# Performance work log

Measured on AMD Instinct MI355X. Metric: run time of the kernel, lower is better.

The kernel has to match this reference:

```python
import jax, jax.numpy as jnp
import numpy as np

B, S, D = 4, 2048, 768
H = 12
HD = D // H  # 64


def setup_inputs() -> dict:
    key = jax.random.key(0)
    ks = jax.random.split(key, 9)
    scale = 0.02
    return {
        "hidden_states": jax.random.normal(ks[0], (B, S, D), dtype=jnp.float32),
        "Wq": jax.random.normal(ks[1], (D, D), dtype=jnp.float32) * scale,
        "bq": jnp.zeros((D,), dtype=jnp.float32),
        "Wk": jax.random.normal(ks[2], (D, D), dtype=jnp.float32) * scale,
        "bk": jnp.zeros((D,), dtype=jnp.float32),
        "Wv": jax.random.normal(ks[3], (D, D), dtype=jnp.float32) * scale,
        "bv": jnp.zeros((D,), dtype=jnp.float32),
        "Wo": jax.random.normal(ks[4], (D, D), dtype=jnp.float32) * scale,
        "bo": jnp.zeros((D,), dtype=jnp.float32),
    }


def reference(hidden_states, Wq, bq, Wk, bk, Wv, bv, Wo, bo):
    b, s, d = hidden_states.shape
    inv_sqrt_hd = 1.0 / jnp.sqrt(jnp.asarray(HD, dtype=hidden_states.dtype))

    def split_heads(x):  # [b, s, d] -> [b, h, s, hd]
        return x.reshape(b, s, H, HD).transpose(0, 2, 1, 3)

    q = split_heads(hidden_states @ Wq + bq)
    k = split_heads(hidden_states @ Wk + bk)
    v = split_heads(hidden_states @ Wv + bv)

    scores = jnp.einsum("bhqd,bhkd->bhqk", q, k) * inv_sqrt_hd
    probs = jax.nn.softmax(scores, axis=-1)
    ctx = jnp.einsum("bhqk,bhkd->bhqd", probs, v)  # [b, h, s, hd]
    ctx = ctx.transpose(0, 2, 1, 3).reshape(b, s, d)
    return ctx @ Wo + bo
```

## Files before the change

### kernel.cpp

```cpp
#include <hip/hip_runtime.h>

typedef unsigned short u16;
typedef __attribute__((ext_vector_type(4))) float f32x4;
typedef __attribute__((ext_vector_type(16))) float f32x16;
typedef __attribute__((ext_vector_type(8))) __bf16 bf16x8;
typedef __attribute__((ext_vector_type(8))) unsigned short u16x8;
typedef __attribute__((ext_vector_type(2))) unsigned u32x2;

#define L2E 1.44269504088896340736f

#if __has_builtin(__builtin_amdgcn_exp2f)
#define EXP2(x) __builtin_amdgcn_exp2f(x)
#else
#define EXP2(x) exp2f(x)
#endif

__device__ __forceinline__ u16 f2bf(float f) {
  unsigned u = __float_as_uint(f);
  u += 0x7fffu + ((u >> 16) & 1u);
  return (u16)(u >> 16);
}

__device__ __forceinline__ unsigned pk2(float a, float b) {
  __bf16 x = (__bf16)a, y = (__bf16)b;
  unsigned short ux = __builtin_bit_cast(unsigned short, x);
  unsigned short uy = __builtin_bit_cast(unsigned short, y);
  return (unsigned)ux | ((unsigned)uy << 16);
}

__device__ __forceinline__ bf16x8 as_bf(uint4 v) { return __builtin_bit_cast(bf16x8, v); }

__device__ __forceinline__ u32x2 plswap(unsigned a, unsigned b) {
#if __has_builtin(__builtin_amdgcn_permlane32_swap)
  auto t = __builtin_amdgcn_permlane32_swap(a, b, false, false);
  return __builtin_bit_cast(u32x2, t);
#else
  unsigned pa = (unsigned)__shfl_xor((int)a, 32, 64);
  unsigned pb = (unsigned)__shfl_xor((int)b, 32, 64);
  const bool hi = (threadIdx.x & 32) != 0;
  u32x2 r;
  r.x = hi ? pb : a;
  r.y = hi ? b : pa;
  return r;
#endif
}

__device__ __forceinline__ void gl2lds16(const void* g, void* l) {
  __builtin_amdgcn_global_load_lds((const __attribute__((address_space(1))) void*)g,
                                   (__attribute__((address_space(3))) void*)l, 16, 0, 0);
}

__global__ void prep(const float* __restrict__ hs, const float* __restrict__ Wq,
                     const float* __restrict__ Wk, const float* __restrict__ Wv,
                     const float* __restrict__ Wo, u16* __restrict__ hsb,
                     u16* __restrict__ wt, u16* __restrict__ wot) {
  const int blk = blockIdx.x;
  const int tid = threadIdx.x;
  if (blk < 6144) {
    const int i = blk * 256 + tid;
    float4 v = ((const float4*)hs)[i];
    ushort4 o;
    o.x = f2bf(v.x); o.y = f2bf(v.y); o.z = f2bf(v.z); o.w = f2bf(v.w);
    ((ushort4*)hsb)[i] = o;
    return;
  }
  __shared__ float ts[32][33];
  const int idx = blk - 6144;
  const int w = idx / 576;
  const int rem = idx % 576;
  const int n0 = (rem % 24) * 32, k0 = (rem / 24) * 32;
  const float* src = (w == 0) ? Wq : (w == 1) ? Wk : (w == 2) ? Wv : Wo;
  u16* dst = (w < 3) ? (wt + (size_t)w * 768 * 768) : wot;
  const float scale = (w == 0) ? 0.125f * L2E : 1.0f;
  const int tx = tid & 31, ty = tid >> 5;
#pragma unroll
  for (int j = 0; j < 4; ++j)
    ts[ty + 8 * j][tx] = src[(size_t)(k0 + ty + 8 * j) * 768 + n0 + tx];
  __syncthreads();
#pragma unroll
  for (int j = 0; j < 4; ++j)
    dst[(size_t)(n0 + ty + 8 * j) * 768 + k0 + tx] = f2bf(ts[tx][ty + 8 * j] * scale);
}

template <int MODE>
__global__ void gemm_bt(const u16* __restrict__ A, const u16* __restrict__ Bt,
                        const float* __restrict__ b0, const float* __restrict__ b1,
                        const float* __restrict__ b2, void* __restrict__ Cout,
                        int M, int N, int K, int nbx) {
  __shared__ u16 As[3][128 * 32];
  __shared__ u16 Bs[3][128 * 32];
  const int tid = threadIdx.x;
  const int lane = tid & 63, wid = tid >> 6;
  const int wr = wid >> 1, wc = wid & 1;
  const int l15 = lane & 15, lg = lane >> 4;
  const int lgx = lg ^ ((l15 >> 1) & 3);

  const int nwg = gridDim.x;
  const int cpx = nwg >> 3;
  const int p = blockIdx.x;
  const int wg = (p & 7) * cpx + (p >> 3);
  const int mblk = (wg / nbx) * 128, nblk = (wg % nbx) * 128;

  f32x4 acc[4][4] = {};

  const int srow = lane >> 2;
  const int skc = ((lane & 3) ^ ((srow >> 1) & 3)) * 8;
  const int rr0 = 32 * wid, rr1 = 32 * wid + 16;

  const u16* ap0 = A + (size_t)(mblk + rr0 + srow) * K + skc;
  const u16* ap1 = A + (size_t)(mblk + rr1 + srow) * K + skc;
  const u16* bp0 = Bt + (size_t)(nblk + rr0 + srow) * K + skc;
  const u16* bp1 = Bt + (size_t)(nblk + rr1 + srow) * K + skc;

#define GSTAGE(buf)                             \
  {                                             \
    gl2lds16(ap0, &As[buf][rr0 * 32]);          \
    gl2lds16(ap1, &As[buf][rr1 * 32]);          \
    gl2lds16(bp0, &Bs[buf][rr0 * 32]);          \
    gl2lds16(bp1, &Bs[buf][rr1 * 32]);          \
    ap0 += 32; ap1 += 32; bp0 += 32; bp1 += 32; \
  }

  const int nt = K >> 5;
  GSTAGE(0);
  GSTAGE(1);
  asm volatile("s_waitcnt vmcnt(4)" ::: "memory");
  __builtin_amdgcn_s_barrier();
  __builtin_amdgcn_sched_barrier(0);

  int cur = 0, stg = 2;
#pragma unroll 1
  for (int t = 0; t < nt; ++t) {
    const bool more = (t + 2 < nt);
    if (more) GSTAGE(stg);
    bf16x8 af[4], bfr[4];
#pragma unroll
    for (int i = 0; i < 4; ++i) {
      af[i] = as_bf(*(const uint4*)&As[cur][(64 * wr + 16 * i + l15) * 32 + 8 * lgx]);
      bfr[i] = as_bf(*(const uint4*)&Bs[cur][(64 * wc + 16 * i + l15) * 32 + 8 * lgx]);
    }
    __builtin_amdgcn_s_setprio(1);
#pragma unroll
    for (int mi = 0; mi < 4; ++mi)
#pragma unroll
      for (int ni = 0; ni < 4; ++ni)
        acc[mi][ni] = __builtin_amdgcn_mfma_f32_16x16x32_bf16(af[mi], bfr[ni], acc[mi][ni], 0, 0, 0);
    __builtin_amdgcn_s_setprio(0);
    if (more)
      asm volatile("s_waitcnt vmcnt(4)" ::: "memory");
    else
      asm volatile("s_waitcnt vmcnt(0)" ::: "memory");
    __builtin_amdgcn_s_barrier();
    __builtin_amdgcn_sched_barrier(0);
    cur = (cur == 2) ? 0 : cur + 1;
    stg = (stg == 2) ? 0 : stg + 1;
  }
#undef GSTAGE

#pragma unroll
  for (int ni = 0; ni < 4; ++ni) {
    const int col = nblk + 64 * wc + 16 * ni + l15;
    float bias;
    if (MODE == 0) {
      if (col < 768) bias = b0[col] * (0.125f * L2E);
      else if (col < 1536) bias = b1[col - 768];
      else bias = b2[col - 1536];
    } else {
      bias = b0[col];
    }
#pragma unroll
    for (int mi = 0; mi < 4; ++mi) {
#pragma unroll
      for (int r = 0; r < 4; ++r) {
        const int row = mblk + 64 * wr + 16 * mi + 4 * lg + r;
        const float v = acc[mi][ni][r] + bias;
        if (MODE == 0)
          ((u16*)Cout)[(size_t)row * N + col] = f2bf(v);
        else
          ((float*)Cout)[(size_t)row * N + col] = v;
      }
    }
  }
}

__global__ void tr_v(const u16* __restrict__ qkv, u16* __restrict__ vt) {
  __shared__ u16 t[64][72];
  const int tid = threadIdx.x;
  const int st = blockIdx.x, h = blockIdx.y, b = blockIdx.z;
  const u16* vsrc = qkv + (size_t)b * 2048 * 2304 + 1536 + h * 64;
  const int s0 = st * 64;
#pragma unroll
  for (int i = 0; i < 2; ++i) {
    const int seg = tid + 256 * i;
    const int row = seg >> 3, slot = seg & 7;
    *(uint4*)&t[row][slot * 8] = *(const uint4*)(vsrc + (size_t)(s0 + row) * 2304 + slot * 8);
  }
  __syncthreads();
  u16* dst = vt + (size_t)(b * 12 + h) * 64 * 2048;
#pragma unroll
  for (int i = 0; i < 2; ++i) {
    const int seg = tid + 256 * i;
    const int hd = seg >> 3, j0 = (seg & 7) * 8;
    u16x8 o;
#pragma unroll
    for (int j = 0; j < 8; ++j) o[j] = t[j0 + j][hd];
    *(u16x8*)(dst + (size_t)hd * 2048 + s0 + j0) = o;
  }
}

__global__ void __launch_bounds__(256, 3)
attn_fwd(const u16* __restrict__ qkv, const u16* __restrict__ vt, u16* __restrict__ ctx) {
  __shared__ u16 Ks[2][64 * 64];
  __shared__ u16 Vs[2][64 * 64];

  const int tid = threadIdx.x;
  const int lane = tid & 63, wid = tid >> 6;
  const int l31 = lane & 31, H = lane >> 5;
  const int r7 = l31 & 7;

  const int p = blockIdx.x;
  const int l = 96 * (p & 7) + (p >> 3);
  const int qb = l & 15;
  const int hb = l >> 4;
  const int h = hb % 12;
  const int b = hb / 12;

  const u16* qbase = qkv + (size_t)b * 2048 * 2304 + h * 64;
  const u16* kbase = qbase + 768;
  const u16* vbase = vt + (size_t)(b * 12 + h) * 64 * 2048;

  const int srow = tid >> 3;
  const int sx = (tid & 7) ^ (srow & 7);
  const int dseg = (tid & ~63) * 8;

  const u16* kp0 = kbase + (size_t)srow * 2304 + 8 * sx;
  const u16* kp1 = kbase + (size_t)(srow + 32) * 2304 + 8 * sx;
  const u16* vp0 = vbase + (size_t)srow * 2048 + 8 * sx;
  const u16* vp1 = vbase + (size_t)(srow + 32) * 2048 + 8 * sx;

  unsigned koff[2][4];
#pragma unroll
  for (int t32 = 0; t32 < 2; ++t32)
#pragma unroll
    for (int ks = 0; ks < 4; ++ks)
      koff[t32][ks] = (32 * t32 + l31) * 64 + 8 * ((2 * ks + H) ^ r7);

  const int q0 = qb * 128 + wid * 32;
  bf16x8 qf[4];
#pragma unroll
  for (int ks = 0; ks < 4; ++ks)
    qf[ks] = as_bf(*(const uint4*)(qbase + (size_t)(q0 + l31) * 2304 + 16 * ks + 8 * H));

  float lsum = 0.f;
  f32x16 o[2] = {};

#define STAGE(buf)                              \
  {                                             \
    gl2lds16(kp0, &Ks[buf][dseg]);              \
    gl2lds16(kp1, &Ks[buf][dseg + 2048]);       \
    gl2lds16(vp0, &Vs[buf][dseg]);              \
    gl2lds16(vp1, &Vs[buf][dseg + 2048]);       \
    kp0 += 64 * 2304; kp1 += 64 * 2304;         \
    vp0 += 64; vp1 += 64;                       \
  }

#define PHASE(CUR)                                                                        \
  {                                                                                       \
    f32x16 st[2] = {};                                                                    \
    __builtin_amdgcn_s_setprio(1);                                                        \
    _Pragma("unroll") for (int k32 = 0; k32 < 2; ++k32)                                   \
        _Pragma("unroll") for (int ks = 0; ks < 4; ++ks) {                                \
      bf16x8 kf = as_bf(*(const uint4*)&Ks[CUR][koff[k32][ks]]);                          \
      st[k32] = __builtin_amdgcn_mfma_f32_32x32x16_bf16(kf, qf[ks], st[k32], 0, 0, 0);    \
    }                                                                                     \
    __builtin_amdgcn_s_setprio(0);                                                        \
                                                         \
    float s0 = 0.f, s1 = 0.f, s2 = 0.f, s3 = 0.f;                                         \
    _Pragma("unroll") for (int k32 = 0; k32 < 2; ++k32)                                   \
        _Pragma("unroll") for (int r = 0; r < 16; r += 4) {                               \
      float e0 = EXP2(st[k32][r + 0]);                                                    \
      float e1 = EXP2(st[k32][r + 1]);                                                    \
      float e2 = EXP2(st[k32][r + 2]);                                                    \
      float e3 = EXP2(st[k32][r + 3]);                                                    \
      st[k32][r + 0] = e0; st[k32][r + 1] = e1;                                           \
      st[k32][r + 2] = e2; st[k32][r + 3] = e3;                                           \
      s0 += e0; s1 += e1; s2 += e2; s3 += e3;                                             \
    }                                                                                     \
    lsum += (s0 + s1) + (s2 + s3);                                                        \
                                              \
    bf16x8 pf[4];                                                                         \
    _Pragma("unroll") for (int ks = 0; ks < 4; ++ks) {                                    \
      const int k32 = ks >> 1, rb = 8 * (ks & 1);                                         \
      unsigned a0 = pk2(st[k32][rb + 0], st[k32][rb + 1]);                                \
      unsigned a1 = pk2(st[k32][rb + 2], st[k32][rb + 3]);                                \
      unsigned a2 = pk2(st[k32][rb + 4], st[k32][rb + 5]);                                \
      unsigned a3 = pk2(st[k32][rb + 6], st[k32][rb + 7]);                                \
      u32x2 s02 = plswap(a0, a2);                                                         \
      u32x2 s13 = plswap(a1, a3);                                                         \
      uint4 w;                                                                            \
      w.x = s02.x; w.y = s13.x; w.z = s02.y; w.w = s13.y;                                 \
      pf[ks] = as_bf(w);                                                                  \
    }                                                                                     \
                                                                      \
    __builtin_amdgcn_s_setprio(1);                                                        \
    _Pragma("unroll") for (int d32 = 0; d32 < 2; ++d32)                                   \
        _Pragma("unroll") for (int ks = 0; ks < 4; ++ks) {                                \
      bf16x8 vf = as_bf(*(const uint4*)&Vs[CUR][koff[d32][ks]]);                          \
      o[d32] = __builtin_amdgcn_mfma_f32_32x32x16_bf16(vf, pf[ks], o[d32], 0, 0, 0);      \
    }                                                                                     \
    __builtin_amdgcn_s_setprio(0);                                                        \
    __syncthreads();                                                                      \
  }

  STAGE(0);
  __syncthreads();

#pragma unroll 1
  for (int cc = 0; cc < 16; ++cc) {
    const int c2 = 2 * cc;
    STAGE(1);
    PHASE(0);
    if (c2 + 2 < 32) STAGE(0);
    PHASE(1);
  }
#undef PHASE
#undef STAGE

  const float ls = lsum + __shfl_xor(lsum, 32, 64);
  const float inv = 1.0f / ls;
  const size_t rowoff = ((size_t)b * 2048 + q0 + l31) * 768 + h * 64;
#pragma unroll
  for (int d32 = 0; d32 < 2; ++d32)
#pragma unroll
    for (int g = 0; g < 4; ++g) {
      uint2 w;
      w.x = pk2(o[d32][4 * g + 0] * inv, o[d32][4 * g + 1] * inv);
      w.y = pk2(o[d32][4 * g + 2] * inv, o[d32][4 * g + 3] * inv);
      *(uint2*)&ctx[rowoff + 32 * d32 + 8 * g + 4 * H] = w;
    }
}

extern "C" void kernel_launch(void* const* d_in, const int* in_sizes, int n_in,
                              void* d_out, int out_size, void* d_ws, size_t ws_size,
                              hipStream_t stream) {
  const float* hs = (const float*)d_in[0];
  const float* Wq = (const float*)d_in[1];
  const float* bq = (const float*)d_in[2];
  const float* Wk = (const float*)d_in[3];
  const float* bk = (const float*)d_in[4];
  const float* Wv = (const float*)d_in[5];
  const float* bv = (const float*)d_in[6];
  const float* Wo = (const float*)d_in[7];
  const float* bo = (const float*)d_in[8];

  char* ws = (char*)d_ws;
  u16* hsb = (u16*)ws;
  u16* wt  = (u16*)(ws + 12582912);
  u16* wot = (u16*)(ws + 16121856);
  u16* qkv = (u16*)(ws + 17301504);
  u16* vt  = (u16*)(ws + 55050240);
  u16* ctx = (u16*)(ws + 67633152);

  prep<<<dim3(8448), dim3(256), 0, stream>>>(hs, Wq, Wk, Wv, Wo, hsb, wt, wot);
  gemm_bt<0><<<dim3(18 * 64), dim3(256), 0, stream>>>(hsb, wt, bq, bk, bv, (void*)qkv,
                                                      8192, 2304, 768, 18);
  tr_v<<<dim3(32, 12, 4), dim3(256), 0, stream>>>(qkv, vt);
  attn_fwd<<<dim3(768), dim3(256), 0, stream>>>(qkv, vt, ctx);
  gemm_bt<1><<<dim3(6 * 64), dim3(256), 0, stream>>>(ctx, wot, bo, bo, bo, d_out,
                                                     8192, 768, 768, 6);
}
```

Baseline: 151.3 us.

## Split attention key range into two halves with a separate combine kernel

```diff
diff --git a/kernel.cpp b/kernel.cpp
--- a/kernel.cpp
+++ b/kernel.cpp
@@ -23,6 +23,13 @@
 
 __device__ __forceinline__ unsigned pk2(float a, float b) {
   __bf16 x = (__bf16)a, y = (__bf16)b;
+  unsigned short ux = __builtin_bit_cast(unsigned short, x);
+  unsigned short uy = __builtin_bit_cast(unsigned short, y);
+  return (unsigned)ux | ((unsigned)uy << 16);
+}
+
+__device__ __forceinline__ unsigned pk2h(float a, float b) {
+  _Float16 x = (_Float16)a, y = (_Float16)b;
   unsigned short ux = __builtin_bit_cast(unsigned short, x);
   unsigned short uy = __builtin_bit_cast(unsigned short, y);
   return (unsigned)ux | ((unsigned)uy << 16);
@@ -209,7 +216,9 @@
 }
 
 __global__ void __launch_bounds__(256, 3)
-attn_fwd(const u16* __restrict__ qkv, const u16* __restrict__ vt, u16* __restrict__ ctx) {
+attn_fwd(const u16* __restrict__ qkv, const u16* __restrict__ vt,
+         u16* __restrict__ p0, u16* __restrict__ p1,
+         float* __restrict__ ls0, float* __restrict__ ls1) {
   __shared__ u16 Ks[2][64 * 64];
   __shared__ u16 Vs[2][64 * 64];
 
@@ -219,9 +228,10 @@
   const int r7 = l31 & 7;
 
   const int p = blockIdx.x;
-  const int l = 96 * (p & 7) + (p >> 3);
+  const int l = 192 * (p & 7) + (p >> 3);
   const int qb = l & 15;
-  const int hb = l >> 4;
+  const int kh = (l >> 4) & 1;
+  const int hb = l >> 5;
   const int h = hb % 12;
   const int b = hb / 12;
 
@@ -233,10 +243,10 @@
   const int sx = (tid & 7) ^ (srow & 7);
   const int dseg = (tid & ~63) * 8;
 
-  const u16* kp0 = kbase + (size_t)srow * 2304 + 8 * sx;
-  const u16* kp1 = kbase + (size_t)(srow + 32) * 2304 + 8 * sx;
-  const u16* vp0 = vbase + (size_t)srow * 2048 + 8 * sx;
-  const u16* vp1 = vbase + (size_t)(srow + 32) * 2048 + 8 * sx;
+  const u16* kp0 = kbase + (size_t)(kh * 1024 + srow) * 2304 + 8 * sx;
+  const u16* kp1 = kbase + (size_t)(kh * 1024 + srow + 32) * 2304 + 8 * sx;
+  const u16* vp0 = vbase + (size_t)srow * 2048 + kh * 1024 + 8 * sx;
+  const u16* vp1 = vbase + (size_t)(srow + 32) * 2048 + kh * 1024 + 8 * sx;
 
   unsigned koff[2][4];
 #pragma unroll
@@ -274,7 +284,6 @@
       st[k32] = __builtin_amdgcn_mfma_f32_32x32x16_bf16(kf, qf[ks], st[k32], 0, 0, 0);    \
     }                                                                                     \
     __builtin_amdgcn_s_setprio(0);                                                        \
-                                                         \
     float s0 = 0.f, s1 = 0.f, s2 = 0.f, s3 = 0.f;                                         \
     _Pragma("unroll") for (int k32 = 0; k32 < 2; ++k32)                                   \
         _Pragma("unroll") for (int r = 0; r < 16; r += 4) {                               \
@@ -287,7 +296,6 @@
       s0 += e0; s1 += e1; s2 += e2; s3 += e3;                                             \
     }                                                                                     \
     lsum += (s0 + s1) + (s2 + s3);                                                        \
-                                              \
     bf16x8 pf[4];                                                                         \
     _Pragma("unroll") for (int ks = 0; ks < 4; ++ks) {                                    \
       const int k32 = ks >> 1, rb = 8 * (ks & 1);                                         \
@@ -301,7 +309,6 @@
       w.x = s02.x; w.y = s13.x; w.z = s02.y; w.w = s13.y;                                 \
       pf[ks] = as_bf(w);                                                                  \
     }                                                                                     \
-                                                                      \
     __builtin_amdgcn_s_setprio(1);                                                        \
     _Pragma("unroll") for (int d32 = 0; d32 < 2; ++d32)                                   \
         _Pragma("unroll") for (int ks = 0; ks < 4; ++ks) {                                \
@@ -316,28 +323,53 @@
   __syncthreads();
 
 #pragma unroll 1
-  for (int cc = 0; cc < 16; ++cc) {
+  for (int cc = 0; cc < 8; ++cc) {
     const int c2 = 2 * cc;
     STAGE(1);
     PHASE(0);
-    if (c2 + 2 < 32) STAGE(0);
+    if (c2 + 2 < 16) STAGE(0);
     PHASE(1);
   }
 #undef PHASE
 #undef STAGE
 
   const float ls = lsum + __shfl_xor(lsum, 32, 64);
-  const float inv = 1.0f / ls;
+  u16* po = kh ? p1 : p0;
+  float* lsb = kh ? ls1 : ls0;
   const size_t rowoff = ((size_t)b * 2048 + q0 + l31) * 768 + h * 64;
 #pragma unroll
   for (int d32 = 0; d32 < 2; ++d32)
 #pragma unroll
     for (int g = 0; g < 4; ++g) {
       uint2 w;
-      w.x = pk2(o[d32][4 * g + 0] * inv, o[d32][4 * g + 1] * inv);
-      w.y = pk2(o[d32][4 * g + 2] * inv, o[d32][4 * g + 3] * inv);
-      *(uint2*)&ctx[rowoff + 32 * d32 + 8 * g + 4 * H] = w;
+      w.x = pk2h(o[d32][4 * g + 0], o[d32][4 * g + 1]);
+      w.y = pk2h(o[d32][4 * g + 2], o[d32][4 * g + 3]);
+      *(uint2*)&po[rowoff + 32 * d32 + 8 * g + 4 * H] = w;
     }
+  if (!H) lsb[((size_t)b * 12 + h) * 2048 + q0 + l31] = ls;
+}
+
+__global__ void combine(const u16* __restrict__ p0, const float* __restrict__ ls0,
+                        const float* __restrict__ ls1, u16* __restrict__ p1ctx) {
+  const int gid = blockIdx.x * 256 + threadIdx.x;
+  const int row = gid / 96;
+  const int c8 = gid - row * 96;
+  const int h = c8 >> 3;
+  const size_t lidx = ((size_t)(row >> 11) * 12 + h) * 2048 + (row & 2047);
+  const float inv = 1.0f / (ls0[lidx] + ls1[lidx]);
+  const size_t e = (size_t)gid * 8;
+  uint4 a = *(const uint4*)(p0 + e);
+  uint4 c = *(const uint4*)(p1ctx + e);
+  const u16* pa = (const u16*)&a;
+  const u16* pc = (const u16*)&c;
+  u16x8 outv;
+#pragma unroll
+  for (int j = 0; j < 8; ++j) {
+    const float s = (float)__builtin_bit_cast(_Float16, pa[j]) +
+                    (float)__builtin_bit_cast(_Float16, pc[j]);
+    outv[j] = f2bf(s * inv);
+  }
+  *(u16x8*)(p1ctx + e) = outv;
 }
 
 extern "C" void kernel_launch(void* const* d_in, const int* in_sizes, int n_in,
@@ -361,11 +393,17 @@
   u16* vt  = (u16*)(ws + 55050240);
   u16* ctx = (u16*)(ws + 67633152);
 
+  u16* p0 = hsb;
+  float* ls0 = (float*)(ws + 12582912);
+  float* ls1 = (float*)(ws + 12582912 + 524288);
+  u16* p1 = ctx;
+
   prep<<<dim3(8448), dim3(256), 0, stream>>>(hs, Wq, Wk, Wv, Wo, hsb, wt, wot);
   gemm_bt<0><<<dim3(18 * 64), dim3(256), 0, stream>>>(hsb, wt, bq, bk, bv, (void*)qkv,
                                                       8192, 2304, 768, 18);
   tr_v<<<dim3(32, 12, 4), dim3(256), 0, stream>>>(qkv, vt);
-  attn_fwd<<<dim3(768), dim3(256), 0, stream>>>(qkv, vt, ctx);
+  attn_fwd<<<dim3(1536), dim3(256), 0, stream>>>(qkv, vt, p0, p1, ls0, ls1);
+  combine<<<dim3(3072), dim3(256), 0, stream>>>(p0, ls0, ls1, p1);
   gemm_bt<1><<<dim3(6 * 64), dim3(256), 0, stream>>>(ctx, wot, bo, bo, bo, d_out,
                                                      8192, 768, 768, 6);
 }
```

New measurement: 159.1 us. 1.05x slower.

## Replace 128x128 GEMM with 256x256 tile, 512-thread double-buffered GEMM

Applied to the files above, without the earlier changes.

```diff
diff --git a/kernel.cpp b/kernel.cpp
--- a/kernel.cpp
+++ b/kernel.cpp
@@ -83,83 +83,98 @@
 }
 
 template <int MODE>
-__global__ void gemm_bt(const u16* __restrict__ A, const u16* __restrict__ Bt,
-                        const float* __restrict__ b0, const float* __restrict__ b1,
-                        const float* __restrict__ b2, void* __restrict__ Cout,
-                        int M, int N, int K, int nbx) {
-  __shared__ u16 As[3][128 * 32];
-  __shared__ u16 Bs[3][128 * 32];
+__global__ void __launch_bounds__(512, 2)
+gemm256(const u16* __restrict__ A, const u16* __restrict__ Bt,
+        const float* __restrict__ b0, const float* __restrict__ b1,
+        const float* __restrict__ b2, void* __restrict__ Cout,
+        int M, int N, int K, int nbx) {
+  extern __shared__ u16 lds[];
   const int tid = threadIdx.x;
   const int lane = tid & 63, wid = tid >> 6;
-  const int wr = wid >> 1, wc = wid & 1;
+  const int wm = wid >> 2, wn = wid & 3;
   const int l15 = lane & 15, lg = lane >> 4;
-  const int lgx = lg ^ ((l15 >> 1) & 3);
+  const int r7 = l15 & 7;
 
   const int nwg = gridDim.x;
   const int cpx = nwg >> 3;
   const int p = blockIdx.x;
   const int wg = (p & 7) * cpx + (p >> 3);
-  const int mblk = (wg / nbx) * 128, nblk = (wg % nbx) * 128;
-
-  f32x4 acc[4][4] = {};
-
-  const int srow = lane >> 2;
-  const int skc = ((lane & 3) ^ ((srow >> 1) & 3)) * 8;
-  const int rr0 = 32 * wid, rr1 = 32 * wid + 16;
-
-  const u16* ap0 = A + (size_t)(mblk + rr0 + srow) * K + skc;
-  const u16* ap1 = A + (size_t)(mblk + rr1 + srow) * K + skc;
-  const u16* bp0 = Bt + (size_t)(nblk + rr0 + srow) * K + skc;
-  const u16* bp1 = Bt + (size_t)(nblk + rr1 + srow) * K + skc;
-
-#define GSTAGE(buf)                             \
-  {                                             \
-    gl2lds16(ap0, &As[buf][rr0 * 32]);          \
-    gl2lds16(ap1, &As[buf][rr1 * 32]);          \
-    gl2lds16(bp0, &Bs[buf][rr0 * 32]);          \
-    gl2lds16(bp1, &Bs[buf][rr1 * 32]);          \
-    ap0 += 32; ap1 += 32; bp0 += 32; bp1 += 32; \
-  }
-
-  const int nt = K >> 5;
-  GSTAGE(0);
-  GSTAGE(1);
-  asm volatile("s_waitcnt vmcnt(4)" ::: "memory");
+  const int mblk = (wg / nbx) * 256, nblk = (wg % nbx) * 256;
+
+  f32x4 acc[8][4] = {};
+
+  const int srow = tid >> 3;
+  const int sx = (tid & 7) ^ (srow & 7);
+  const u16* Ag = A + (size_t)(mblk + srow) * K + 8 * sx;
+  const u16* Bg = Bt + (size_t)(nblk + srow) * K + 8 * sx;
+
+#define STA(ob, skt, j) \
+  gl2lds16(Ag + (size_t)(j) * 64 * K + (size_t)(skt) * 64, lds + (ob) * 32768 + (j) * 4096 + tid * 8)
+#define STB(ob, skt, j) \
+  gl2lds16(Bg + (size_t)(j) * 64 * K + (size_t)(skt) * 64, lds + (ob) * 32768 + 16384 + (j) * 4096 + tid * 8)
+
+  const int sl0 = 8 * (lg ^ r7);
+  const int sl1 = 8 * ((4 + lg) ^ r7);
+  const int arb = (wm * 128 + l15) * 64;
+  const int brb = (wn * 64 + l15) * 64;
+
+#define GROUP(bb, dost, skt)                                                                 \
+  {                                                                                          \
+    bf16x8 af[4][2], bfr[2][2];                                                              \
+    _Pragma("unroll") for (int ph = 0; ph < 4; ++ph) {                                       \
+      const int mh = ph >> 1, nh = ph & 1;                                                   \
+      if (nh == 0) {                                                                         \
+        _Pragma("unroll") for (int m = 0; m < 4; ++m) {                                      \
+          af[m][0] = as_bf(*(const uint4*)&lds[(bb) * 32768 + arb + mh * 4096 + m * 1024 + sl0]); \
+          af[m][1] = as_bf(*(const uint4*)&lds[(bb) * 32768 + arb + mh * 4096 + m * 1024 + sl1]); \
+        }                                                                                    \
+      }                                                                                      \
+      _Pragma("unroll") for (int n = 0; n < 2; ++n) {                                        \
+        bfr[n][0] = as_bf(*(const uint4*)&lds[(bb) * 32768 + 16384 + brb + nh * 2048 + n * 1024 + sl0]); \
+        bfr[n][1] = as_bf(*(const uint4*)&lds[(bb) * 32768 + 16384 + brb + nh * 2048 + n * 1024 + sl1]); \
+      }                                                                                      \
+      if (dost) {                                                                            \
+        if (ph == 0) { STA(bb ^ 1, skt, 0); STA(bb ^ 1, skt, 1); }                           \
+        if (ph == 1) { STA(bb ^ 1, skt, 2); STA(bb ^ 1, skt, 3); }                           \
+        if (ph == 2) { STB(bb ^ 1, skt, 0); STB(bb ^ 1, skt, 1); }                           \
+        if (ph == 3) { STB(bb ^ 1, skt, 2); STB(bb ^ 1, skt, 3); }                           \
+      }                                                                                      \
+      __builtin_amdgcn_s_barrier();                                                          \
+      __builtin_amdgcn_s_setprio(1);                                                         \
+      _Pragma("unroll") for (int m = 0; m < 4; ++m)                                          \
+        _Pragma("unroll") for (int n = 0; n < 2; ++n) {                                      \
+          acc[mh * 4 + m][nh * 2 + n] = __builtin_amdgcn_mfma_f32_16x16x32_bf16(             \
+              af[m][0], bfr[n][0], acc[mh * 4 + m][nh * 2 + n], 0, 0, 0);                    \
+          acc[mh * 4 + m][nh * 2 + n] = __builtin_amdgcn_mfma_f32_16x16x32_bf16(             \
+              af[m][1], bfr[n][1], acc[mh * 4 + m][nh * 2 + n], 0, 0, 0);                    \
+        }                                                                                    \
+      __builtin_amdgcn_s_setprio(0);                                                         \
+      if (ph == 3) asm volatile("s_waitcnt vmcnt(0)" ::: "memory");                          \
+      __builtin_amdgcn_s_barrier();                                                          \
+    }                                                                                        \
+    __builtin_amdgcn_sched_barrier(0);                                                       \
+  }
+
+#pragma unroll
+  for (int j = 0; j < 4; ++j) { STA(0, 0, j); STB(0, 0, j); }
+  asm volatile("s_waitcnt vmcnt(0)" ::: "memory");
   __builtin_amdgcn_s_barrier();
   __builtin_amdgcn_sched_barrier(0);
 
-  int cur = 0, stg = 2;
+  const int nt = K >> 6;
 #pragma unroll 1
-  for (int t = 0; t < nt; ++t) {
-    const bool more = (t + 2 < nt);
-    if (more) GSTAGE(stg);
-    bf16x8 af[4], bfr[4];
-#pragma unroll
-    for (int i = 0; i < 4; ++i) {
-      af[i] = as_bf(*(const uint4*)&As[cur][(64 * wr + 16 * i + l15) * 32 + 8 * lgx]);
-      bfr[i] = as_bf(*(const uint4*)&Bs[cur][(64 * wc + 16 * i + l15) * 32 + 8 * lgx]);
-    }
-    __builtin_amdgcn_s_setprio(1);
-#pragma unroll
-    for (int mi = 0; mi < 4; ++mi)
-#pragma unroll
-      for (int ni = 0; ni < 4; ++ni)
-        acc[mi][ni] = __builtin_amdgcn_mfma_f32_16x16x32_bf16(af[mi], bfr[ni], acc[mi][ni], 0, 0, 0);
-    __builtin_amdgcn_s_setprio(0);
-    if (more)
-      asm volatile("s_waitcnt vmcnt(4)" ::: "memory");
-    else
-      asm volatile("s_waitcnt vmcnt(0)" ::: "memory");
-    __builtin_amdgcn_s_barrier();
-    __builtin_amdgcn_sched_barrier(0);
-    cur = (cur == 2) ? 0 : cur + 1;
-    stg = (stg == 2) ? 0 : stg + 1;
-  }
-#undef GSTAGE
+  for (int it = 0; it < (nt >> 1); ++it) {
+    GROUP(0, true, 2 * it + 1);
+    const bool more = (2 * it + 2) < nt;
+    GROUP(1, more, 2 * it + 2);
+  }
+#undef GROUP
+#undef STA
+#undef STB
 
 #pragma unroll
   for (int ni = 0; ni < 4; ++ni) {
-    const int col = nblk + 64 * wc + 16 * ni + l15;
+    const int col = nblk + wn * 64 + 16 * ni + l15;
     float bias;
     if (MODE == 0) {
       if (col < 768) bias = b0[col] * (0.125f * L2E);
@@ -169,10 +184,10 @@
       bias = b0[col];
     }
 #pragma unroll
-    for (int mi = 0; mi < 4; ++mi) {
+    for (int mi = 0; mi < 8; ++mi) {
 #pragma unroll
       for (int r = 0; r < 4; ++r) {
-        const int row = mblk + 64 * wr + 16 * mi + 4 * lg + r;
+        const int row = mblk + wm * 128 + 16 * mi + 4 * lg + r;
         const float v = acc[mi][ni][r] + bias;
         if (MODE == 0)
           ((u16*)Cout)[(size_t)row * N + col] = f2bf(v);
@@ -274,7 +289,6 @@
       st[k32] = __builtin_amdgcn_mfma_f32_32x32x16_bf16(kf, qf[ks], st[k32], 0, 0, 0);    \
     }                                                                                     \
     __builtin_amdgcn_s_setprio(0);                                                        \
-                                                         \
     float s0 = 0.f, s1 = 0.f, s2 = 0.f, s3 = 0.f;                                         \
     _Pragma("unroll") for (int k32 = 0; k32 < 2; ++k32)                                   \
         _Pragma("unroll") for (int r = 0; r < 16; r += 4) {                               \
@@ -287,7 +301,6 @@
       s0 += e0; s1 += e1; s2 += e2; s3 += e3;                                             \
     }                                                                                     \
     lsum += (s0 + s1) + (s2 + s3);                                                        \
-                                              \
     bf16x8 pf[4];                                                                         \
     _Pragma("unroll") for (int ks = 0; ks < 4; ++ks) {                                    \
       const int k32 = ks >> 1, rb = 8 * (ks & 1);                                         \
@@ -301,7 +314,6 @@
       w.x = s02.x; w.y = s13.x; w.z = s02.y; w.w = s13.y;                                 \
       pf[ks] = as_bf(w);                                                                  \
     }                                                                                     \
-                                                                      \
     __builtin_amdgcn_s_setprio(1);                                                        \
     _Pragma("unroll") for (int d32 = 0; d32 < 2; ++d32)                                   \
         _Pragma("unroll") for (int ks = 0; ks < 4; ++ks) {                                \
@@ -362,10 +374,10 @@
   u16* ctx = (u16*)(ws + 67633152);
 
   prep<<<dim3(8448), dim3(256), 0, stream>>>(hs, Wq, Wk, Wv, Wo, hsb, wt, wot);
-  gemm_bt<0><<<dim3(18 * 64), dim3(256), 0, stream>>>(hsb, wt, bq, bk, bv, (void*)qkv,
-                                                      8192, 2304, 768, 18);
+  gemm256<0><<<dim3(288), dim3(512), 131072, stream>>>(hsb, wt, bq, bk, bv, (void*)qkv,
+                                                       8192, 2304, 768, 9);
   tr_v<<<dim3(32, 12, 4), dim3(256), 0, stream>>>(qkv, vt);
   attn_fwd<<<dim3(768), dim3(256), 0, stream>>>(qkv, vt, ctx);
-  gemm_bt<1><<<dim3(6 * 64), dim3(256), 0, stream>>>(ctx, wot, bo, bo, bo, d_out,
-                                                     8192, 768, 768, 6);
-}
+  gemm256<1><<<dim3(96), dim3(512), 131072, stream>>>(ctx, wot, bo, bo, bo, d_out,
+                                                      8192, 768, 768, 3);
+}
```

New measurement: 218.9 us. 1.45x slower.
